# Kernel optimization log

Measured on AMD Instinct MI355X. Metric: run time of the kernel, lower is better.

Reference implementation:

```python
import jax, jax.numpy as jnp
from jax import lax
import numpy as np

# ---- static config (matches init_kwargs) ----
B, H, W = 8, 32, 32
L = H * W                      # 1024 tokens
D_MODEL = 384
MAMBA_DIM = 192                # d_model * d_mamba_ratio
LOCAL_DIM = 192
D_INNER = 384                  # expand_m * MAMBA_DIM
D_STATE = 16
D_CONV = 4
DT_RANK = 12                   # ceil(MAMBA_DIM / 16)
NDIR = 4                       # h, h_flip, v, v_flip
RED = 48                       # int(D_INNER * 0.125), BiAttn reduce dim
INNER_C = 192                  # LOCAL_DIM * expand_c
K_C = 8                        # local block depthwise kernel size


def setup_inputs() -> dict:
    key = jax.random.key(0)
    ks = jax.random.split(key, 16)
    s = 0.02
    return {
        "x": jax.random.normal(ks[0], (B, L, D_MODEL), jnp.float32),
        "in_proj_w": jax.random.normal(ks[1], (2 * D_INNER, MAMBA_DIM)) * s,
        "A_log": jnp.broadcast_to(jnp.log(jnp.arange(1, D_STATE + 1, dtype=jnp.float32)), (NDIR, D_INNER, D_STATE)) + 0.0,
        "conv_w": jax.random.normal(ks[2], (NDIR, D_INNER, D_CONV)) * 0.2,
        "conv_b": jax.random.normal(ks[3], (NDIR, D_INNER)) * 0.02,
        "xproj_w": jax.random.normal(ks[4], (NDIR, DT_RANK + 2 * D_STATE, D_INNER)) * s,
        "dtproj_w": jax.random.normal(ks[5], (NDIR, D_INNER, DT_RANK)) * (DT_RANK ** -0.5),
        "dtproj_b": jax.random.normal(ks[6], (NDIR, D_INNER)) * 0.5 - 4.0,
        "Dp": jnp.ones((NDIR, D_INNER)),
        "out_proj_w": jax.random.normal(ks[7], (MAMBA_DIM, D_INNER)) * s,
        "attn_ln_g": jnp.ones((D_INNER,)),
        "attn_ln_b": jnp.zeros((D_INNER,)),
        "attn_gr_w": jax.random.normal(ks[8], (RED, D_INNER)) * s,
        "attn_gr_b": jnp.zeros((RED,)),
        "attn_cs_w": jax.random.normal(ks[9], (D_INNER, RED)) * s,
        "attn_cs_b": jnp.zeros((D_INNER,)),
        "pw1_w": jax.random.normal(ks[10], (2 * INNER_C, LOCAL_DIM)) * s,
        "pw1_b": jnp.zeros((2 * INNER_C,)),
        "dw_w": jax.random.normal(ks[11], (INNER_C, K_C)) * 0.2,
        "dw_b": jnp.zeros((INNER_C,)),
        "bn_g": jnp.ones((INNER_C,)),
        "bn_b": jnp.zeros((INNER_C,)),
        "pw2_w": jax.random.normal(ks[12], (LOCAL_DIM, INNER_C)) * s,
        "pw2_b": jnp.zeros((LOCAL_DIM,)),
    }


def _forward(x, in_proj_w, A_log, conv_w, conv_b, xproj_w, dtproj_w, dtproj_b, Dp,
             out_proj_w, attn_ln_g, attn_ln_b, attn_gr_w, attn_gr_b, attn_cs_w, attn_cs_b,
             pw1_w, pw1_b, dw_w, dw_b, bn_g, bn_b, pw2_w, pw2_b):
    mamba_in = x[:, :, :MAMBA_DIM]
    local_in = x[:, :, MAMBA_DIM:]

    # ---------- MultiMamba branch ----------
    xz = jnp.swapaxes(mamba_in @ in_proj_w.T, 1, 2)   # (B, 2*D_INNER, L)

    def to_dir(t, i):
        # reorder channel-last-token axis per scan direction
        if i == 0:
            return t
        if i == 1:
            return jnp.flip(t, -1)
        tv = t.reshape(B, -1, H, W).swapaxes(-1, -2).reshape(B, -1, L)  # column-major scan
        return tv if i == 2 else jnp.flip(tv, -1)

    def from_dir(t, i):
        if i == 0:
            return t
        if i == 1:
            return jnp.flip(t, -1)
        if i == 3:
            t = jnp.flip(t, -1)
        return t.reshape(B, -1, W, H).swapaxes(-1, -2).reshape(B, -1, L)

    def ssm_dir(xzd, i):
        # mamba_inner_fn_no_out_proj: causal dwconv -> silu -> x_proj -> selective scan -> gate
        xp, z = jnp.split(xzd, 2, axis=1)            # (B, D_INNER, L) each
        xpad = jnp.pad(xp, ((0, 0), (0, 0), (D_CONV - 1, 0)))
        u = lax.conv_general_dilated(xpad, conv_w[i][:, None, :], (1,), 'VALID',
                                     dimension_numbers=('NCH', 'OIH', 'NCH'),
                                     feature_group_count=D_INNER)
        u = jax.nn.silu(u + conv_b[i][None, :, None])
        dbl = jnp.einsum('bdl,rd->brl', u, xproj_w[i])
        dt = dbl[:, :DT_RANK]
        Bm = dbl[:, DT_RANK:DT_RANK + D_STATE]
        Cm = dbl[:, DT_RANK + D_STATE:]
        delta = jax.nn.softplus(jnp.einsum('brl,dr->bdl', dt, dtproj_w[i]) + dtproj_b[i][None, :, None])
        A = -jnp.exp(A_log[i])                        # (D_INNER, D_STATE)

        def step(h, inps):
            d_t, B_t, C_t, u_t = inps                 # (B,d),(B,n),(B,n),(B,d)
            h = jnp.exp(d_t[:, :, None] * A) * h + (d_t * u_t)[:, :, None] * B_t[:, None, :]
            return h, jnp.einsum('bdn,bn->bd', h, C_t)

        h0 = jnp.zeros((B, D_INNER, D_STATE), x.dtype)
        _, ys = lax.scan(step, h0, (delta.transpose(2, 0, 1), Bm.transpose(2, 0, 1),
                                    Cm.transpose(2, 0, 1), u.transpose(2, 0, 1)))
        y = ys.transpose(1, 2, 0) + u * Dp[i][:, None]  # (B, D_INNER, L)
        return y * jax.nn.silu(z)

    def biattn(t):                                     # (B, L, D_INNER)
        mu = t.mean(-1, keepdims=True)
        var = ((t - mu) ** 2).mean(-1, keepdims=True)
        tn = (t - mu) / jnp.sqrt(var + 1e-5) * attn_ln_g + attn_ln_b
        g = tn.mean(1, keepdims=True)                  # global pool (B,1,D_INNER)
        g = jax.nn.gelu(g @ attn_gr_w.T + attn_gr_b, approximate=False)
        c = jax.nn.sigmoid(g @ attn_cs_w.T + attn_cs_b)
        return t * c

    acc = jnp.zeros((B, L, D_INNER), x.dtype)
    for i in range(NDIR):                              # fixed small set of directions
        out_i = from_dir(ssm_dir(to_dir(xz, i), i), i)
        acc = acc + biattn(jnp.swapaxes(out_i, 1, 2))
    mamba_out = acc @ out_proj_w.T                     # (B, L, MAMBA_DIM)

    # ---------- Local conv branch ----------
    hch = jnp.einsum('blc,oc->bol', local_in, pw1_w) + pw1_b[None, :, None]
    a, gte = jnp.split(hch, 2, axis=1)
    hch = a * jax.nn.sigmoid(gte)                      # GLU, (B, INNER_C, L)
    pad_l = K_C // 2
    pad_r = K_C // 2 - (K_C + 1) % 2                   # calc_same_padding(8) -> (4, 3)
    hpad = jnp.pad(hch, ((0, 0), (0, 0), (pad_l, pad_r)))
    hch = lax.conv_general_dilated(hpad, dw_w[:, None, :], (1,), 'VALID',
                                   dimension_numbers=('NCH', 'OIH', 'NCH'),
                                   feature_group_count=INNER_C) + dw_b[None, :, None]
    mu = hch.mean((0, 2))                              # BatchNorm1d (training-mode batch stats)
    var = hch.var((0, 2))
    hch = (hch - mu[None, :, None]) / jnp.sqrt(var + 1e-5)[None, :, None] * bn_g[None, :, None] + bn_b[None, :, None]
    hch = hch * jax.nn.sigmoid(hch)                    # Swish
    local_out = jnp.einsum('bcl,oc->blo', hch, pw2_w) + pw2_b

    return jnp.concatenate([mamba_out, local_out], axis=-1)


def reference(x, in_proj_w, A_log, conv_w, conv_b, xproj_w, dtproj_w, dtproj_b, Dp,
              out_proj_w, attn_ln_g, attn_ln_b, attn_gr_w, attn_gr_b, attn_cs_w, attn_cs_b,
              pw1_w, pw1_b, dw_w, dw_b, bn_g, bn_b, pw2_w, pw2_b):
    return _forward(x, in_proj_w, A_log, conv_w, conv_b, xproj_w, dtproj_w, dtproj_b, Dp,
                    out_proj_w, attn_ln_g, attn_ln_b, attn_gr_w, attn_gr_b, attn_cs_w, attn_cs_b,
                    pw1_w, pw1_b, dw_w, dw_b, bn_g, bn_b, pw2_w, pw2_b)
```

## Files before the change

### kernel.cpp

```cpp
#include <hip/hip_runtime.h>
#include <stdint.h>


#define DEV __device__ __forceinline__

typedef __attribute__((ext_vector_type(8))) short short8;
typedef __attribute__((ext_vector_type(4))) short short4v;
typedef __attribute__((ext_vector_type(4))) float f32x4;

DEV float bf(ushort v) { union { uint32_t u; float f; } c; c.u = ((uint32_t)v) << 16; return c.f; }
DEV ushort fbf(float f) {
  union { float f; uint32_t u; } c; c.f = f;
  uint32_t u = c.u;
  return (ushort)((u + 0x7FFFu + ((u >> 16) & 1u)) >> 16);
}

#if __has_builtin(__builtin_amdgcn_exp2f)
DEV float fexp2(float x) { return __builtin_amdgcn_exp2f(x); }
#else
DEV float fexp2(float x) { return __expf(x * 0.6931471805599453f); }
#endif

template<int CTRL>
DEV float rradd(float x) {
  return x + __int_as_float(__builtin_amdgcn_update_dpp(
      0, __float_as_int(x), CTRL, 0xF, 0xF, true));
}

DEV int pmap(int i, int j) {
  if (i == 0) return j;
  if (i == 1) return 1023 - j;
  if (i == 2) return ((j & 31) << 5) | (j >> 5);
  int k = 1023 - j; return ((k & 31) << 5) | (k >> 5);
}

DEV void cvt4(const float* __restrict__ s, ushort* __restrict__ d, int blk, int tid) {
  const int idx = (blk * 256 + tid) * 4;
  float4 v = *(const float4*)(s + idx);
  d[idx] = fbf(v.x); d[idx + 1] = fbf(v.y); d[idx + 2] = fbf(v.z); d[idx + 3] = fbf(v.w);
}

__global__ __launch_bounds__(256) void prep_all(
    const float* __restrict__ x, ushort* __restrict__ xb,
    const float* __restrict__ ipw, ushort* __restrict__ ipwb,
    const float* __restrict__ opw, ushort* __restrict__ opwb,
    const float* __restrict__ pw1w, ushort* __restrict__ pw1wb,
    const float* __restrict__ pw2w, ushort* __restrict__ pw2wb,
    const float* __restrict__ xw, ushort* __restrict__ xwp)
{
  const int bx = blockIdx.x, tid = threadIdx.x;
  if (bx < 3072)      cvt4(x, xb, bx, tid);
  else if (bx < 3216) cvt4(ipw, ipwb, bx - 3072, tid);
  else if (bx < 3288) cvt4(opw, opwb, bx - 3216, tid);
  else if (bx < 3360) cvt4(pw1w, pw1wb, bx - 3288, tid);
  else if (bx < 3396) cvt4(pw2w, pw2wb, bx - 3360, tid);
  else {
    const int row = bx - 3396;
    const int i = row >> 6, nn = row & 63;
    for (int c = tid; c < 384; c += 256)
      xwp[(size_t)row * 384 + c] = (nn < 44) ? fbf(xw[((size_t)i * 44 + nn) * 384 + c]) : (ushort)0;
  }
}

template<bool BF16OUT, bool BIAS>
__global__ __launch_bounds__(256) void gemm_bt(
    const ushort* __restrict__ A, long long sAz, int lda,
    const ushort* __restrict__ Bw, long long sBz,
    const float* __restrict__ bias,
    void* __restrict__ C, long long sCz, int ldc, int coff, int K)
{
  __shared__ ushort As[64][40];
  __shared__ ushort Bs[64][40];
  A += (size_t)blockIdx.z * sAz;
  Bw += (size_t)blockIdx.z * sBz;
  const int tid = threadIdx.x;
  const int m0 = blockIdx.x * 64, n0 = blockIdx.y * 64;
  const int w = tid >> 6, lane = tid & 63, l15 = lane & 15, quad = lane >> 4;
  const int sr = tid >> 2, sc = (tid & 3) * 8;
  f32x4 acc[4] = {};
  for (int k0 = 0; k0 < K; k0 += 32) {
    __syncthreads();
    *(short8*)&As[sr][sc] = *(const short8*)(A + (size_t)(m0 + sr) * lda + k0 + sc);
    *(short8*)&Bs[sr][sc] = *(const short8*)(Bw + (size_t)(n0 + sr) * K + k0 + sc);
    __syncthreads();
    short8 av = *(short8*)&As[w * 16 + l15][quad * 8];
#pragma unroll
    for (int nt = 0; nt < 4; nt++) {
      short8 bv = *(short8*)&Bs[nt * 16 + l15][quad * 8];
      acc[nt] = __builtin_amdgcn_mfma_f32_16x16x32_bf16(av, bv, acc[nt], 0, 0, 0);
    }
  }
  float* cf = (float*)C + (size_t)blockIdx.z * sCz;
  ushort* cb = (ushort*)C + (size_t)blockIdx.z * sCz;
#pragma unroll
  for (int nt = 0; nt < 4; nt++) {
    const int col = n0 + nt * 16 + l15;
    const float bv = BIAS ? bias[col] : 0.f;
#pragma unroll
    for (int r = 0; r < 4; r++) {
      const int row = m0 + w * 16 + quad * 4 + r;
      float v = acc[nt][r] + bv;
      if (BF16OUT) cb[(size_t)row * ldc + coff + col] = fbf(v);
      else         cf[(size_t)row * ldc + coff + col] = v;
    }
  }
}

__global__ __launch_bounds__(256) void gemm_dual(
    const ushort* __restrict__ A0, int lda0, const ushort* __restrict__ B0,
    const float* __restrict__ bias0, void* __restrict__ C0, int ldc0, int coff0, int K0,
    int nt0, int bf0,
    const ushort* __restrict__ A1, int lda1, const ushort* __restrict__ B1,
    const float* __restrict__ bias1, void* __restrict__ C1, int ldc1, int coff1, int K1,
    int bf1)
{
  __shared__ ushort As[64][40];
  __shared__ ushort Bs[64][40];
  const ushort* A; const ushort* Bw; const float* bias; void* C;
  int lda, ldc, coff, K, bf16o, n0;
  if ((int)blockIdx.y < nt0) {
    A = A0; lda = lda0; Bw = B0; bias = bias0; C = C0; ldc = ldc0; coff = coff0; K = K0;
    bf16o = bf0; n0 = blockIdx.y * 64;
  } else {
    A = A1; lda = lda1; Bw = B1; bias = bias1; C = C1; ldc = ldc1; coff = coff1; K = K1;
    bf16o = bf1; n0 = (blockIdx.y - nt0) * 64;
  }
  const int tid = threadIdx.x;
  const int m0 = blockIdx.x * 64;
  const int w = tid >> 6, lane = tid & 63, l15 = lane & 15, quad = lane >> 4;
  const int sr = tid >> 2, sc = (tid & 3) * 8;
  f32x4 acc[4] = {};
  for (int k0 = 0; k0 < K; k0 += 32) {
    __syncthreads();
    *(short8*)&As[sr][sc] = *(const short8*)(A + (size_t)(m0 + sr) * lda + k0 + sc);
    *(short8*)&Bs[sr][sc] = *(const short8*)(Bw + (size_t)(n0 + sr) * K + k0 + sc);
    __syncthreads();
    short8 av = *(short8*)&As[w * 16 + l15][quad * 8];
#pragma unroll
    for (int nt = 0; nt < 4; nt++) {
      short8 bv = *(short8*)&Bs[nt * 16 + l15][quad * 8];
      acc[nt] = __builtin_amdgcn_mfma_f32_16x16x32_bf16(av, bv, acc[nt], 0, 0, 0);
    }
  }
#pragma unroll
  for (int nt = 0; nt < 4; nt++) {
    const int col = n0 + nt * 16 + l15;
    const float bv = bias ? bias[col] : 0.f;
#pragma unroll
    for (int r = 0; r < 4; r++) {
      const int row = m0 + w * 16 + quad * 4 + r;
      float v = acc[nt][r] + bv;
      if (bf16o) ((ushort*)C)[(size_t)row * ldc + coff + col] = fbf(v);
      else       ((float*)C)[(size_t)row * ldc + coff + col] = v;
    }
  }
}

__global__ __launch_bounds__(256) void gemm_pw2(
    const float* __restrict__ h2, const float* __restrict__ bnsum,
    const float* __restrict__ bng, const float* __restrict__ bnb,
    const ushort* __restrict__ Bw, const float* __restrict__ bias,
    float* __restrict__ C)
{
  __shared__ ushort As[64][40];
  __shared__ ushort Bs[64][40];
  __shared__ float bsc[192], bsh[192];
  const int tid = threadIdx.x;
  const int m0 = blockIdx.x * 64, n0 = blockIdx.y * 64;
  const int w = tid >> 6, lane = tid & 63, l15 = lane & 15, quad = lane >> 4;
  const int sr = tid >> 2, sc = (tid & 3) * 8;
  for (int cth = tid; cth < 192; cth += 256) {
    float m = bnsum[cth] * (1.f / 8192.f);
    float va = bnsum[192 + cth] * (1.f / 8192.f) - m * m;
    float s = bng[cth] * rsqrtf(va + 1e-5f);
    bsc[cth] = s; bsh[cth] = bnb[cth] - m * s;
  }
  f32x4 acc[4] = {};
  for (int k0 = 0; k0 < 192; k0 += 32) {
    __syncthreads();
    {
      const float* hr = h2 + (size_t)(m0 + sr) * 192 + k0 + sc;
      f32x4 a0 = *(const f32x4*)(hr);
      f32x4 a1 = *(const f32x4*)(hr + 4);
      short8 v;
#pragma unroll
      for (int k = 0; k < 8; k++) {
        const float xx = (k < 4) ? a0[k] : a1[k - 4];
        const float xn = xx * bsc[k0 + sc + k] + bsh[k0 + sc + k];
        v[k] = (short)fbf(xn / (1.f + __expf(-xn)));
      }
      *(short8*)&As[sr][sc] = v;
    }
    *(short8*)&Bs[sr][sc] = *(const short8*)(Bw + (size_t)(n0 + sr) * 192 + k0 + sc);
    __syncthreads();
    short8 av = *(short8*)&As[w * 16 + l15][quad * 8];
#pragma unroll
    for (int nt = 0; nt < 4; nt++) {
      short8 bv = *(short8*)&Bs[nt * 16 + l15][quad * 8];
      acc[nt] = __builtin_amdgcn_mfma_f32_16x16x32_bf16(av, bv, acc[nt], 0, 0, 0);
    }
  }
#pragma unroll
  for (int nt = 0; nt < 4; nt++) {
    const int col = n0 + nt * 16 + l15;
    const float bv = bias[col];
#pragma unroll
    for (int r = 0; r < 4; r++) {
      const int row = m0 + w * 16 + quad * 4 + r;
      C[(size_t)row * 384 + 192 + col] = acc[nt][r] + bv;
    }
  }
}

__global__ __launch_bounds__(384) void conv2_kernel(const ushort* __restrict__ xzb,
    const float* __restrict__ cw, const float* __restrict__ cb, ushort* __restrict__ u)
{
  const int d = threadIdx.x;
  const int jt = blockIdx.x;
  const int b = blockIdx.y, i = blockIdx.z;
  __shared__ ushort sx[35][384];
  const int j0 = jt * 32;
#pragma unroll 5
  for (int r = 0; r < 35; r++) {
    const int jj = j0 - 3 + r;
    sx[r][d] = (jj >= 0) ? xzb[(size_t)((b << 10) + pmap(i, jj)) * 768 + d] : (ushort)0;
  }
  __syncthreads();
  const float w0 = cw[((i * 384 + d) << 2) + 0];
  const float w1 = cw[((i * 384 + d) << 2) + 1];
  const float w2 = cw[((i * 384 + d) << 2) + 2];
  const float w3 = cw[((i * 384 + d) << 2) + 3];
  const float cbv = cb[i * 384 + d];
  ushort* ur = u + ((size_t)((i * 8 + b) << 10) + j0) * 384 + d;
#pragma unroll 4
  for (int q = 0; q < 32; q++) {
    float s = bf(sx[q][d]) * w0 + bf(sx[q + 1][d]) * w1 + bf(sx[q + 2][d]) * w2
            + bf(sx[q + 3][d]) * w3 + cbv;
    ur[(size_t)q * 384] = fbf(s / (1.f + __expf(-s)));
  }
}

#define NCH 16
#define CJ 64
__global__ __launch_bounds__(256, 3) void scan9_kernel(
    const ushort* __restrict__ u,
    const float*  __restrict__ dbl,
    const ushort* __restrict__ xzb,
    const float* __restrict__ alog, const float* __restrict__ dtw,
    const float* __restrict__ dtb, const float* __restrict__ Dpw,
    ushort* __restrict__ y)
{
  const int dt0 = blockIdx.x * NCH;
  const int b = blockIdx.y, i = blockIdx.z;
  const int tid = threadIdx.x;
  const int ch = tid >> 4, n = tid & 15;
  const int srow = tid >> 2, role = tid & 3;

  __shared__ float sbc[CJ / 2][68];
  __shared__ float sdu[CJ / 2][68];
  __shared__ float sy[CJ][20];
  __shared__ float sDp[NCH];

  float w48[4][12], dtbv4[4];
#pragma unroll
  for (int cc = 0; cc < 4; cc++) {
    const int chp = 4 * role + cc;
#pragma unroll
    for (int r = 0; r < 12; r++) w48[cc][r] = dtw[((size_t)i * 384 + dt0 + chp) * 12 + r];
    dtbv4[cc] = dtb[i * 384 + dt0 + chp];
  }
  const float L2E = 1.4426950408889634f;
  const float Al = -__expf(alog[((size_t)i * 384 + dt0 + ch) * 16 + n]) * L2E;
  if (tid < NCH) sDp[tid] = Dpw[i * 384 + dt0 + tid];

  const float selm[4] = { (n >> 2) == 0 ? 1.f : 0.f, (n >> 2) == 1 ? 1.f : 0.f,
                          (n >> 2) == 2 ? 1.f : 0.f, (n >> 2) == 3 ? 1.f : 0.f };

  const size_t rb = (size_t)(i * 8 + b) << 10;
  const ushort* ub = u + rb * 384 + dt0;
  const float* dblb = dbl + rb * 64;
  const ushort* zb = xzb + ((size_t)b << 10) * 768 + 384 + dt0;
  ushort* yb = y + rb * 384 + dt0;
  const float* sdup = &sdu[0][4 * ch];
  const float* sbcp = &sbc[0][4 * n];

  f32x4 nd0, nd1, nd2, ns0, ns1, ns2; short4v nu, nz;
  {
    const float* src = dblb + (size_t)srow * 64;
    nd0 = *(const f32x4*)(src); nd1 = *(const f32x4*)(src + 4); nd2 = *(const f32x4*)(src + 8);
    const float* seg = src + role * 12;
    ns0 = *(const f32x4*)(seg); ns1 = *(const f32x4*)(seg + 4); ns2 = *(const f32x4*)(seg + 8);
    nu = *(const short4v*)(ub + (size_t)srow * 384 + 4 * role);
    nz = *(const short4v*)(zb + (size_t)pmap(i, srow) * 768 + 4 * role);
  }

  float h = 0.f;

  for (int c = 0; c < 16; c++) {
    const int j0 = c * CJ;
    f32x4 uf, zf;
#pragma unroll
    for (int k = 0; k < 4; k++) { uf[k] = bf((ushort)nu[k]); zf[k] = bf((ushort)nz[k]); }
    if (role != 0) {
      float vals[12];
#pragma unroll
      for (int k = 0; k < 4; k++) { vals[k] = ns0[k]; vals[4 + k] = ns1[k]; vals[8 + k] = ns2[k]; }
#pragma unroll
      for (int k = 0; k < 12; k++) {
        const int f = role * 12 + k;
        if (f < 44) {
          const int isC = (f >= 28) ? 1 : 0;
          const int nn = isC ? (f - 28) : (f - 12);
          sbc[srow >> 1][4 * nn + 2 * (srow & 1) + isC] = vals[k];
        }
      }
    }
    {
      float dtr[12];
#pragma unroll
      for (int k = 0; k < 4; k++) { dtr[k] = nd0[k]; dtr[4 + k] = nd1[k]; dtr[8 + k] = nd2[k]; }
#pragma unroll
      for (int cc = 0; cc < 4; cc++) {
        float s = dtbv4[cc];
#pragma unroll
        for (int r = 0; r < 12; r++) s += dtr[r] * w48[cc][r];
        const float dl = fmaxf(s, 0.f) + __logf(1.f + __expf(-fabsf(s)));
        float2 pr; pr.x = dl; pr.y = dl * uf[cc];
        *(float2*)&sdu[srow >> 1][4 * (4 * role + cc) + 2 * (srow & 1)] = pr;
      }
    }
    __syncthreads();
    {
      const int cn = (c < 15) ? (c + 1) : 0;
      const int rown = cn * CJ + srow;
      const float* src = dblb + (size_t)rown * 64;
      nd0 = *(const f32x4*)(src); nd1 = *(const f32x4*)(src + 4); nd2 = *(const f32x4*)(src + 8);
      const float* seg = src + role * 12;
      ns0 = *(const f32x4*)(seg); ns1 = *(const f32x4*)(seg + 4); ns2 = *(const f32x4*)(seg + 8);
      nu = *(const short4v*)(ub + (size_t)rown * 384 + 4 * role);
      nz = *(const short4v*)(zb + (size_t)pmap(i, rown) * 768 + 4 * role);
    }
#pragma unroll
    for (int q = 0; q < 4; q++) {
      f32x4 pq = {0.f, 0.f, 0.f, 0.f};
#pragma unroll
      for (int s2 = 0; s2 < 8; s2++) {
        const f32x4 duP = *(const f32x4*)(sdup + (q * 8 + s2) * 68);
        const f32x4 bcP = *(const f32x4*)(sbcp + (q * 8 + s2) * 68);
        {
          const float e = fexp2(duP[0] * Al);
          h = e * h + duP[1] * bcP[0];
          float p = h * bcP[1];
          p = rradd<0x124>(p); p = rradd<0x128>(p);
          pq[s2 >> 1] = fmaf(selm[(2 * s2) & 3], p, pq[s2 >> 1]);
        }
        {
          const float e = fexp2(duP[2] * Al);
          h = e * h + duP[3] * bcP[2];
          float p = h * bcP[3];
          p = rradd<0x124>(p); p = rradd<0x128>(p);
          pq[s2 >> 1] = fmaf(selm[(2 * s2 + 1) & 3], p, pq[s2 >> 1]);
        }
      }
#pragma unroll
      for (int j = 0; j < 4; j++) {
        float t2 = rradd<0xB1>(pq[j]);
        t2 = rradd<0x4E>(t2);
        if ((n & 3) == 0) sy[(q << 4) | (j << 2) | (n >> 2)][ch] = t2;
      }
    }
    __syncthreads();
    {
      const int lo = pmap(i, j0 + srow);
      const f32x4 y4 = *(const f32x4*)&sy[srow][role * 4];
      short4v o;
#pragma unroll
      for (int t = 0; t < 4; t++) {
        const float z = zf[t];
        const float val = (y4[t] + uf[t] * sDp[role * 4 + t]) * (z / (1.f + __expf(-z)));
        o[t] = (short)fbf(val);
      }
      *(short4v*)(yb + (size_t)lo * 384 + role * 4) = o;
    }
  }
}

__global__ __launch_bounds__(256) void lngm_kernel(const ushort* __restrict__ y,
                                                   float* __restrict__ G16)
{
  const int slab = blockIdx.x, b = blockIdx.y, i = blockIdx.z;
  const int tid = threadIdx.x;
  const int w = tid >> 6, lane = tid & 63;
  __shared__ float smu[64], srs[64];
  __shared__ ushort sy16[64][384];
  const size_t base = (size_t)i * 8192 + b * 1024 + slab * 64;
  for (int rr = 0; rr < 16; rr++) {
    const int r = w * 16 + rr;
    const ushort* yr = y + (base + r) * 384;
    const short4v v4 = *(const short4v*)(yr + 4 * lane);
    const uint32_t v2 = *(const uint32_t*)(yr + 256 + 2 * lane);
    *(short4v*)&sy16[r][4 * lane] = v4;
    *(uint32_t*)&sy16[r][256 + 2 * lane] = v2;
    float s = 0.f, ss = 0.f;
#pragma unroll
    for (int t = 0; t < 4; t++) { float v = bf((ushort)v4[t]); s += v; ss += v * v; }
    { float v = bf((ushort)(v2 & 0xffffu)); s += v; ss += v * v; }
    { float v = bf((ushort)(v2 >> 16));     s += v; ss += v * v; }
#pragma unroll
    for (int off = 1; off < 64; off <<= 1) { s += __shfl_xor(s, off, 64); ss += __shfl_xor(ss, off, 64); }
    if (lane == 0) {
      float m = s * (1.f / 384.f);
      float va = ss * (1.f / 384.f) - m * m;
      smu[r] = m;
      srs[r] = rsqrtf(va + 1e-5f);
    }
  }
  __syncthreads();
  if (tid < 192) {
    const int c0 = tid * 2;
    float s0 = 0.f, s1 = 0.f;
#pragma unroll 8
    for (int r = 0; r < 64; r++) {
      const uint32_t pv = *(const uint32_t*)&sy16[r][c0];
      const float rs = srs[r], mu = smu[r];
      s0 += (bf((ushort)(pv & 0xffffu)) - mu) * rs;
      s1 += (bf((ushort)(pv >> 16)) - mu) * rs;
    }
    float* g = G16 + ((size_t)(i * 8 + b) * 16 + slab) * 384 + c0;
    g[0] = s0; g[1] = s1;
  }
}

__global__ __launch_bounds__(64) void gate_kernel(const float* __restrict__ G16,
    const float* __restrict__ lng, const float* __restrict__ lnb,
    const float* __restrict__ grw, const float* __restrict__ grb,
    const float* __restrict__ csw, const float* __restrict__ csb, float* __restrict__ cbuf)
{
  const int b = blockIdx.x, i = blockIdx.y;
  const int ib = i * 8 + b;
  const int lane = threadIdx.x;
  __shared__ float sG[384];
  __shared__ float g48[48];
  for (int dd = lane; dd < 384; dd += 64) {
    const float* g = G16 + (size_t)ib * 16 * 384 + dd;
    float s = 0.f;
#pragma unroll
    for (int k = 0; k < 16; k++) s += g[k * 384];
    sG[dd] = s * (1.f / 1024.f) * lng[dd] + lnb[dd];
  }
  __syncthreads();
  if (lane < 48) {
    float s = grb[lane];
    for (int dd = 0; dd < 384; dd++) s += sG[dd] * grw[lane * 384 + dd];
    g48[lane] = 0.5f * s * (1.f + erff(s * 0.70710678118f));
  }
  __syncthreads();
  for (int dd = lane; dd < 384; dd += 64) {
    float s = csb[dd];
#pragma unroll
    for (int r = 0; r < 48; r++) s += g48[r] * csw[dd * 48 + r];
    cbuf[(size_t)ib * 384 + dd] = 1.f / (1.f + __expf(-s));
  }
}

__global__ __launch_bounds__(384) void accgate_kernel(const ushort* __restrict__ y,
    const float* __restrict__ cbuf, ushort* __restrict__ accb)
{
  const int t = threadIdx.x;
  const int row = blockIdx.x * 4 + (t / 96);
  const int cg = (t % 96) * 4;
  const int b = row >> 10;
  f32x4 s = {};
#pragma unroll
  for (int i = 0; i < 4; i++) {
    const short4v v = *(const short4v*)(y + ((size_t)i * 8192 + row) * 384 + cg);
    const f32x4 cv = *(const f32x4*)(cbuf + (size_t)(i * 8 + b) * 384 + cg);
#pragma unroll
    for (int k = 0; k < 4; k++) s[k] += bf((ushort)v[k]) * cv[k];
  }
  short4v o;
#pragma unroll
  for (int k = 0; k < 4; k++) o[k] = (short)fbf(s[k]);
  *(short4v*)(accb + (size_t)row * 384 + cg) = o;
}

__global__ __launch_bounds__(192) void gludwbn_kernel(const ushort* __restrict__ hchb,
    const float* __restrict__ dww, const float* __restrict__ dwb,
    float* __restrict__ h2, float* __restrict__ bnsum)
{
  const int c = threadIdx.x;
  const int lt = blockIdx.x, b = blockIdx.y;
  __shared__ float sv[23][192];
  const int l0 = lt * 16;
#pragma unroll 4
  for (int r = 0; r < 23; r++) {
    const int ls = l0 + r - 4;
    float v = 0.f;
    if (ls >= 0 && ls < 1024) {
      const size_t rr = (size_t)((b << 10) + ls) * 384;
      const float a = bf(hchb[rr + c]);
      const float g = bf(hchb[rr + 192 + c]);
      v = a / (1.f + __expf(-g));
    }
    sv[r][c] = v;
  }
  __syncthreads();
  float wk[8];
#pragma unroll
  for (int k = 0; k < 8; k++) wk[k] = dww[(c << 3) + k];
  const float bias = dwb[c];
  float sacc = 0.f, ssacc = 0.f;
  for (int q = 0; q < 16; q++) {
    float s = bias;
#pragma unroll
    for (int k = 0; k < 8; k++) s += sv[q + k][c] * wk[k];
    h2[(size_t)((b << 10) + l0 + q) * 192 + c] = s;
    sacc += s; ssacc += s * s;
  }
  atomicAdd(&bnsum[c], sacc);
  atomicAdd(&bnsum[192 + c], ssacc);
}

extern "C" void kernel_launch(void* const* d_in, const int* in_sizes, int n_in,
                              void* d_out, int out_size, void* d_ws, size_t ws_size,
                              hipStream_t stream) {
  const float* x    = (const float*)d_in[0];
  const float* ipw  = (const float*)d_in[1];
  const float* alog = (const float*)d_in[2];
  const float* cw   = (const float*)d_in[3];
  const float* cbv  = (const float*)d_in[4];
  const float* xw   = (const float*)d_in[5];
  const float* dtw  = (const float*)d_in[6];
  const float* dtb  = (const float*)d_in[7];
  const float* Dpw  = (const float*)d_in[8];
  const float* opw  = (const float*)d_in[9];
  const float* lng  = (const float*)d_in[10];
  const float* lnb  = (const float*)d_in[11];
  const float* grw  = (const float*)d_in[12];
  const float* grb  = (const float*)d_in[13];
  const float* csw  = (const float*)d_in[14];
  const float* csb  = (const float*)d_in[15];
  const float* pw1w = (const float*)d_in[16];
  const float* pw1b = (const float*)d_in[17];
  const float* dww  = (const float*)d_in[18];
  const float* dwb  = (const float*)d_in[19];
  const float* bng  = (const float*)d_in[20];
  const float* bnb  = (const float*)d_in[21];
  const float* pw2w = (const float*)d_in[22];
  const float* pw2b = (const float*)d_in[23];
  float* out = (float*)d_out;

  char* ws = (char*)d_ws;
  ushort* xb    = (ushort*)(ws + 0);
  ushort* xzb   = (ushort*)(ws + 6291456);
  ushort* u     = (ushort*)(ws + 18874368);
  float*  dbl   = (float*)(ws + 44040192);
  ushort* y     = (ushort*)(ws + 52428800);
  ushort* accb  = (ushort*)(ws + 77594624);
  float*  G16   = (float*)(ws + 83886080);
  float*  cbuf  = (float*)(ws + 84672512);
  ushort* xwp   = (ushort*)(ws + 84721664);
  ushort* ipwb  = (ushort*)(ws + 84918272);
  ushort* opwb  = (ushort*)(ws + 85213184);
  ushort* pw1wb = (ushort*)(ws + 85360640);
  ushort* pw2wb = (ushort*)(ws + 85508096);
  float*  bnsum = (float*)(ws + 85581824);
  ushort* hchb = (ushort*)(ws + 18874368);
  float*  h2   = (float*)(ws + 34603008);

  prep_all<<<dim3(3652), 256, 0, stream>>>(x, xb, ipw, ipwb, opw, opwb,
                                           pw1w, pw1wb, pw2w, pw2wb, xw, xwp);
  gemm_bt<true, false><<<dim3(128, 12, 1), 256, 0, stream>>>(
      xb, 0, 384, ipwb, 0, nullptr, xzb, 0, 768, 0, 192);
  conv2_kernel<<<dim3(32, 8, 4), 384, 0, stream>>>(xzb, cw, cbv, u);
  gemm_bt<false, false><<<dim3(128, 1, 4), 256, 0, stream>>>(
      u, 8192LL * 384, 384, xwp, 64LL * 384, nullptr, dbl, 8192LL * 64, 64, 0, 384);
  scan9_kernel<<<dim3(24, 8, 4), 256, 0, stream>>>(u, dbl, xzb, alog, dtw, dtb, Dpw, y);
  lngm_kernel<<<dim3(16, 8, 4), 256, 0, stream>>>(y, G16);
  gate_kernel<<<dim3(8, 4), 64, 0, stream>>>(G16, lng, lnb, grw, grb, csw, csb, cbuf);
  accgate_kernel<<<dim3(2048), 384, 0, stream>>>(y, cbuf, accb);
  gemm_dual<<<dim3(128, 9), 256, 0, stream>>>(
      accb, 384, opwb, nullptr, out, 384, 0, 384, 3, 0,
      xb + 192, 384, pw1wb, pw1b, hchb, 384, 0, 192, 1);
  (void)hipMemsetAsync(bnsum, 0, 384 * sizeof(float), stream);
  gludwbn_kernel<<<dim3(64, 8), 192, 0, stream>>>(hchb, dww, dwb, h2, bnsum);
  gemm_pw2<<<dim3(128, 3), 256, 0, stream>>>(h2, bnsum, bng, bnb, pw2wb, pw2b, out);
}
```

Measured before the change: 322.7 us.

## Fuse depthwise conv with x_proj GEMM, double-buffer scan output, fold memset

Merges the causal depthwise conv+SiLU kernel and the x_proj GEMM into one kernel. Each block computes 64 rows of u, writes them, then reruns a GEMM over those rows into dbl, reusing the conv shared buffer as the GEMM tiles. The scan kernel double-buffers its shared arrays so each chunk's output epilogue is deferred into the next iteration, removing one barrier per chunk. The bnsum memset moves into the first block of gemm_dual, dropping one launch. The fused kernel reads u back from global memory right after writing it. It also launches only 512 blocks with a large shared-memory footprint, which may reduce parallelism.

```diff
diff --git a/kernel.cpp b/kernel.cpp
--- a/kernel.cpp
+++ b/kernel.cpp
@@ -112,10 +112,13 @@
     int nt0, int bf0,
     const ushort* __restrict__ A1, int lda1, const ushort* __restrict__ B1,
     const float* __restrict__ bias1, void* __restrict__ C1, int ldc1, int coff1, int K1,
-    int bf1)
+    int bf1, float* __restrict__ bnsum)
 {
   __shared__ ushort As[64][40];
   __shared__ ushort Bs[64][40];
+  if (blockIdx.x == 0 && blockIdx.y == 0) {
+    for (int k = threadIdx.x; k < 384; k += 256) bnsum[k] = 0.f;
+  }
   const ushort* A; const ushort* Bw; const float* bias; void* C;
   int lda, ldc, coff, K, bf16o, n0;
   if ((int)blockIdx.y < nt0) {
@@ -212,37 +215,85 @@
   }
 }
 
-__global__ __launch_bounds__(384) void conv2_kernel(const ushort* __restrict__ xzb,
-    const float* __restrict__ cw, const float* __restrict__ cb, ushort* __restrict__ u)
-{
-  const int d = threadIdx.x;
-  const int jt = blockIdx.x;
-  const int b = blockIdx.y, i = blockIdx.z;
-  __shared__ ushort sx[35][384];
-  const int j0 = jt * 32;
-#pragma unroll 5
-  for (int r = 0; r < 35; r++) {
-    const int jj = j0 - 3 + r;
-    sx[r][d] = (jj >= 0) ? xzb[(size_t)((b << 10) + pmap(i, jj)) * 768 + d] : (ushort)0;
+__global__ __launch_bounds__(256) void convdbl_kernel(
+    const ushort* __restrict__ xzb, const float* __restrict__ cw,
+    const float* __restrict__ cb, const ushort* __restrict__ xwp,
+    ushort* __restrict__ u, float* __restrict__ dbl)
+{
+  __shared__ __align__(16) ushort sxz[67][392];
+  __shared__ float swt[384][4];
+  __shared__ float scb[384];
+  const int tid = threadIdx.x;
+  const int i = blockIdx.y;
+  const int m0 = blockIdx.x * 64;
+  const int b = m0 >> 10, j0 = m0 & 1023;
+
+  for (int k = tid; k < 1536; k += 256) ((float*)swt)[k] = cw[(size_t)i * 1536 + k];
+  for (int k = tid; k < 384; k += 256) scb[k] = cb[i * 384 + k];
+  for (int g = tid; g < 67 * 96; g += 256) {
+    const int rr = g / 96, c4 = (g % 96) * 4;
+    const int jj = j0 - 3 + rr;
+    short4v v = {};
+    if (jj >= 0)
+      v = *(const short4v*)(xzb + (size_t)((b << 10) + pmap(i, jj)) * 768 + c4);
+    *(short4v*)&sxz[rr][c4] = v;
   }
   __syncthreads();
-  const float w0 = cw[((i * 384 + d) << 2) + 0];
-  const float w1 = cw[((i * 384 + d) << 2) + 1];
-  const float w2 = cw[((i * 384 + d) << 2) + 2];
-  const float w3 = cw[((i * 384 + d) << 2) + 3];
-  const float cbv = cb[i * 384 + d];
-  ushort* ur = u + ((size_t)((i * 8 + b) << 10) + j0) * 384 + d;
+  {
+    const int r = tid >> 2, cp = tid & 3;
+    ushort* ur = u + ((size_t)((i * 8 + b) << 10) + j0 + r) * 384 + cp * 96;
 #pragma unroll 4
-  for (int q = 0; q < 32; q++) {
-    float s = bf(sx[q][d]) * w0 + bf(sx[q + 1][d]) * w1 + bf(sx[q + 2][d]) * w2
-            + bf(sx[q + 3][d]) * w3 + cbv;
-    ur[(size_t)q * 384] = fbf(s / (1.f + __expf(-s)));
+    for (int q = 0; q < 24; q++) {
+      const int c = cp * 96 + q * 4;
+      const short4v x0 = *(const short4v*)&sxz[r + 0][c];
+      const short4v x1 = *(const short4v*)&sxz[r + 1][c];
+      const short4v x2 = *(const short4v*)&sxz[r + 2][c];
+      const short4v x3 = *(const short4v*)&sxz[r + 3][c];
+      short4v o;
+#pragma unroll
+      for (int j = 0; j < 4; j++) {
+        const f32x4 wv = *(const f32x4*)&swt[c + j][0];
+        float s = bf((ushort)x0[j]) * wv[0] + bf((ushort)x1[j]) * wv[1]
+                + bf((ushort)x2[j]) * wv[2] + bf((ushort)x3[j]) * wv[3] + scb[c + j];
+        o[j] = (short)fbf(s / (1.f + __expf(-s)));
+      }
+      *(short4v*)(ur + q * 4) = o;
+    }
+  }
+  ushort (*As)[40] = (ushort(*)[40])&sxz[0][0];
+  ushort (*Bs)[40] = (ushort(*)[40])(&sxz[0][0] + 2560);
+  const ushort* Au = u + (size_t)i * 8192 * 384;
+  const ushort* Bw = xwp + (size_t)i * 64 * 384;
+  const int w = tid >> 6, lane = tid & 63, l15 = lane & 15, quad = lane >> 4;
+  const int sr = tid >> 2, sc = (tid & 3) * 8;
+  f32x4 acc[4] = {};
+  for (int k0 = 0; k0 < 384; k0 += 32) {
+    __syncthreads();
+    *(short8*)&As[sr][sc] = *(const short8*)(Au + (size_t)(m0 + sr) * 384 + k0 + sc);
+    *(short8*)&Bs[sr][sc] = *(const short8*)(Bw + (size_t)sr * 384 + k0 + sc);
+    __syncthreads();
+    short8 av = *(short8*)&As[w * 16 + l15][quad * 8];
+#pragma unroll
+    for (int nt = 0; nt < 4; nt++) {
+      short8 bv = *(short8*)&Bs[nt * 16 + l15][quad * 8];
+      acc[nt] = __builtin_amdgcn_mfma_f32_16x16x32_bf16(av, bv, acc[nt], 0, 0, 0);
+    }
+  }
+  float* cf = dbl + (size_t)i * 8192 * 64;
+#pragma unroll
+  for (int nt = 0; nt < 4; nt++) {
+    const int col = nt * 16 + l15;
+#pragma unroll
+    for (int r = 0; r < 4; r++) {
+      const int row = m0 + w * 16 + quad * 4 + r;
+      cf[(size_t)row * 64 + col] = acc[nt][r];
+    }
   }
 }
 
 #define NCH 16
 #define CJ 64
-__global__ __launch_bounds__(256, 3) void scan9_kernel(
+__global__ __launch_bounds__(256, 3) void scan9b_kernel(
     const ushort* __restrict__ u,
     const float*  __restrict__ dbl,
     const ushort* __restrict__ xzb,
@@ -256,9 +307,9 @@
   const int ch = tid >> 4, n = tid & 15;
   const int srow = tid >> 2, role = tid & 3;
 
-  __shared__ float sbc[CJ / 2][68];
-  __shared__ float sdu[CJ / 2][68];
-  __shared__ float sy[CJ][20];
+  __shared__ float sbc[2][CJ / 2][68];
+  __shared__ float sdu[2][CJ / 2][68];
+  __shared__ float sy[2][CJ][20];
   __shared__ float sDp[NCH];
 
   float w48[4][12], dtbv4[4];
@@ -281,8 +332,6 @@
   const float* dblb = dbl + rb * 64;
   const ushort* zb = xzb + ((size_t)b << 10) * 768 + 384 + dt0;
   ushort* yb = y + rb * 384 + dt0;
-  const float* sdup = &sdu[0][4 * ch];
-  const float* sbcp = &sbc[0][4 * n];
 
   f32x4 nd0, nd1, nd2, ns0, ns1, ns2; short4v nu, nz;
   {
@@ -295,9 +344,10 @@
   }
 
   float h = 0.f;
+  f32x4 ufp = {}, zfp = {};
 
   for (int c = 0; c < 16; c++) {
-    const int j0 = c * CJ;
+    const int bsel = c & 1;
     f32x4 uf, zf;
 #pragma unroll
     for (int k = 0; k < 4; k++) { uf[k] = bf((ushort)nu[k]); zf[k] = bf((ushort)nz[k]); }
@@ -311,7 +361,7 @@
         if (f < 44) {
           const int isC = (f >= 28) ? 1 : 0;
           const int nn = isC ? (f - 28) : (f - 12);
-          sbc[srow >> 1][4 * nn + 2 * (srow & 1) + isC] = vals[k];
+          sbc[bsel][srow >> 1][4 * nn + 2 * (srow & 1) + isC] = vals[k];
         }
       }
     }
@@ -326,10 +376,22 @@
         for (int r = 0; r < 12; r++) s += dtr[r] * w48[cc][r];
         const float dl = fmaxf(s, 0.f) + __logf(1.f + __expf(-fabsf(s)));
         float2 pr; pr.x = dl; pr.y = dl * uf[cc];
-        *(float2*)&sdu[srow >> 1][4 * (4 * role + cc) + 2 * (srow & 1)] = pr;
+        *(float2*)&sdu[bsel][srow >> 1][4 * (4 * role + cc) + 2 * (srow & 1)] = pr;
       }
     }
     __syncthreads();
+    if (c > 0) {
+      const int lo = pmap(i, (c - 1) * CJ + srow);
+      const f32x4 y4 = *(const f32x4*)&sy[bsel ^ 1][srow][role * 4];
+      short4v o;
+#pragma unroll
+      for (int t = 0; t < 4; t++) {
+        const float z = zfp[t];
+        const float val = (y4[t] + ufp[t] * sDp[role * 4 + t]) * (z / (1.f + __expf(-z)));
+        o[t] = (short)fbf(val);
+      }
+      *(short4v*)(yb + (size_t)lo * 384 + role * 4) = o;
+    }
     {
       const int cn = (c < 15) ? (c + 1) : 0;
       const int rown = cn * CJ + srow;
@@ -340,13 +402,15 @@
       nu = *(const short4v*)(ub + (size_t)rown * 384 + 4 * role);
       nz = *(const short4v*)(zb + (size_t)pmap(i, rown) * 768 + 4 * role);
     }
+    const float* sduc = &sdu[bsel][0][4 * ch];
+    const float* sbcc = &sbc[bsel][0][4 * n];
 #pragma unroll
     for (int q = 0; q < 4; q++) {
       f32x4 pq = {0.f, 0.f, 0.f, 0.f};
 #pragma unroll
       for (int s2 = 0; s2 < 8; s2++) {
-        const f32x4 duP = *(const f32x4*)(sdup + (q * 8 + s2) * 68);
-        const f32x4 bcP = *(const f32x4*)(sbcp + (q * 8 + s2) * 68);
+        const f32x4 duP = *(const f32x4*)(sduc + (q * 8 + s2) * 68);
+        const f32x4 bcP = *(const f32x4*)(sbcc + (q * 8 + s2) * 68);
         {
           const float e = fexp2(duP[0] * Al);
           h = e * h + duP[1] * bcP[0];
@@ -366,22 +430,23 @@
       for (int j = 0; j < 4; j++) {
         float t2 = rradd<0xB1>(pq[j]);
         t2 = rradd<0x4E>(t2);
-        if ((n & 3) == 0) sy[(q << 4) | (j << 2) | (n >> 2)][ch] = t2;
+        if ((n & 3) == 0) sy[bsel][(q << 4) | (j << 2) | (n >> 2)][ch] = t2;
       }
     }
-    __syncthreads();
-    {
-      const int lo = pmap(i, j0 + srow);
-      const f32x4 y4 = *(const f32x4*)&sy[srow][role * 4];
-      short4v o;
-#pragma unroll
-      for (int t = 0; t < 4; t++) {
-        const float z = zf[t];
-        const float val = (y4[t] + uf[t] * sDp[role * 4 + t]) * (z / (1.f + __expf(-z)));
-        o[t] = (short)fbf(val);
-      }
-      *(short4v*)(yb + (size_t)lo * 384 + role * 4) = o;
-    }
+    ufp = uf; zfp = zf;
+  }
+  __syncthreads();
+  {
+    const int lo = pmap(i, 15 * CJ + srow);
+    const f32x4 y4 = *(const f32x4*)&sy[1][srow][role * 4];
+    short4v o;
+#pragma unroll
+    for (int t = 0; t < 4; t++) {
+      const float z = zfp[t];
+      const float val = (y4[t] + ufp[t] * sDp[role * 4 + t]) * (z / (1.f + __expf(-z)));
+      o[t] = (short)fbf(val);
+    }
+    *(short4v*)(yb + (size_t)lo * 384 + role * 4) = o;
   }
 }
 
@@ -572,17 +637,14 @@
                                            pw1w, pw1wb, pw2w, pw2wb, xw, xwp);
   gemm_bt<true, false><<<dim3(128, 12, 1), 256, 0, stream>>>(
       xb, 0, 384, ipwb, 0, nullptr, xzb, 0, 768, 0, 192);
-  conv2_kernel<<<dim3(32, 8, 4), 384, 0, stream>>>(xzb, cw, cbv, u);
-  gemm_bt<false, false><<<dim3(128, 1, 4), 256, 0, stream>>>(
-      u, 8192LL * 384, 384, xwp, 64LL * 384, nullptr, dbl, 8192LL * 64, 64, 0, 384);
-  scan9_kernel<<<dim3(24, 8, 4), 256, 0, stream>>>(u, dbl, xzb, alog, dtw, dtb, Dpw, y);
+  convdbl_kernel<<<dim3(128, 4), 256, 0, stream>>>(xzb, cw, cbv, xwp, u, dbl);
+  scan9b_kernel<<<dim3(24, 8, 4), 256, 0, stream>>>(u, dbl, xzb, alog, dtw, dtb, Dpw, y);
   lngm_kernel<<<dim3(16, 8, 4), 256, 0, stream>>>(y, G16);
   gate_kernel<<<dim3(8, 4), 64, 0, stream>>>(G16, lng, lnb, grw, grb, csw, csb, cbuf);
   accgate_kernel<<<dim3(2048), 384, 0, stream>>>(y, cbuf, accb);
   gemm_dual<<<dim3(128, 9), 256, 0, stream>>>(
       accb, 384, opwb, nullptr, out, 384, 0, 384, 3, 0,
-      xb + 192, 384, pw1wb, pw1b, hchb, 384, 0, 192, 1);
-  (void)hipMemsetAsync(bnsum, 0, 384 * sizeof(float), stream);
+      xb + 192, 384, pw1wb, pw1b, hchb, 384, 0, 192, 1, bnsum);
   gludwbn_kernel<<<dim3(64, 8), 192, 0, stream>>>(hchb, dww, dwb, h2, bnsum);
   gemm_pw2<<<dim3(128, 3), 256, 0, stream>>>(h2, bnsum, bng, bnb, pw2wb, pw2b, out);
 }
```

After: 322.3 us. No clear change (-0.1%).
